# Kernel optimization log

Hardware: AMD Instinct MI355X
Metric: run time of the kernel (lower is better)

Reference implementation:

```python
import jax, jax.numpy as jnp
import numpy as np

DIM = 512
N_DAYS = 24

def setup_inputs() -> dict:
    key = jax.random.key(0)
    k1, k2, k3, k4 = jax.random.split(key, 4)
    x = jax.random.normal(k1, (64, 1024, DIM), dtype=jnp.float32)
    day_ids = jax.random.randint(k2, (64,), 0, N_DAYS, dtype=jnp.int64)
    W = jax.random.normal(k3, (N_DAYS, DIM, DIM), dtype=jnp.float32) * 0.02 + jnp.eye(DIM, dtype=jnp.float32)
    b = jax.random.normal(k4, (N_DAYS, DIM), dtype=jnp.float32) * 0.02
    return {"x": x, "day_ids": day_ids, "W": W, "b": b}

def reference(x, day_ids, W, b):
    # Gather per-sample day weights/biases, batched matmul + bias, softsign.
    # (Dropout is identity in eval mode.)
    Wd = W[day_ids]            # [B, dim, dim]
    bd = b[day_ids][:, None, :]  # [B, 1, dim]
    y = jnp.einsum('btd,bde->bte', x, Wd) + bd
    return y / (1.0 + jnp.abs(y))  # Softsign
```

## Files before the change

kernel.cpp:

```cpp
#include <hip/hip_runtime.h>


#define DIM 512
#define SEQ 1024
#define NB 64
#define NDAYS 24
#define BM 64
#define BN 128
#define BK 64
#define LDA (BK + 8)

typedef __bf16 bf16x8 __attribute__((ext_vector_type(8)));
typedef __bf16 bf16x4 __attribute__((ext_vector_type(4)));
typedef float  f32x4  __attribute__((ext_vector_type(4)));

__device__ __forceinline__ void gll16(const void* g, void* l) {
    __builtin_amdgcn_global_load_lds(
        (const __attribute__((address_space(1))) unsigned int*)g,
        (__attribute__((address_space(3))) unsigned int*)l,
        16, 0, 0);
}

__global__ __launch_bounds__(256)
void transpose_w_kernel(const float* __restrict__ W, __bf16* __restrict__ Wt) {
    __shared__ __bf16 T[32][33];
    const int d  = blockIdx.z;
    const int k0 = blockIdx.x * 32;
    const int n0 = blockIdx.y * 32;
    const int tx = threadIdx.x & 31;
    const int ty = threadIdx.x >> 5;
    const float* Wd = W + (size_t)d * DIM * DIM;
    #pragma unroll
    for (int i = 0; i < 4; ++i) {
        const int k = ty + i * 8;
        T[tx][k] = (__bf16)Wd[(size_t)(k0 + k) * DIM + n0 + tx];
    }
    __syncthreads();
    __bf16* Wtd = Wt + (size_t)d * DIM * DIM;
    #pragma unroll
    for (int i = 0; i < 4; ++i) {
        const int n = ty + i * 8;
        Wtd[(size_t)(n0 + n) * DIM + k0 + tx] = T[n][tx];
    }
}

__global__ __launch_bounds__(256, 5)
void day_adapter_kernel(const float* __restrict__ x,
                        const int*   __restrict__ day_ids,
                        const __bf16* __restrict__ Wt,
                        const float* __restrict__ bias,
                        float*       __restrict__ out)
{
    __shared__ __align__(16) __bf16 As[BM][LDA];
    __shared__ __align__(16) __bf16 Bs[BN * BK];

    const int L  = blockIdx.x;
    const int g  = (L >> 3) & 3;
    const int mb = (L & 7) | ((L >> 5) << 3);
    const int m  = mb & 15;
    const int bb = mb >> 4;

    const int n0  = g * BN;
    const int m0  = m * BM;
    const int tid = threadIdx.x;
    const int day = day_ids[bb];

    const float*  xb  = x   + (size_t)bb  * SEQ * DIM + (size_t)m0 * DIM;
    const __bf16* Wtb = Wt  + (size_t)day * DIM * DIM + (size_t)n0 * DIM;
    float*        ob  = out + (size_t)bb  * SEQ * DIM + (size_t)m0 * DIM + n0;

    const int wave = tid >> 6;
    const int lane = tid & 63;
    const int wm   = (wave >> 1) * 32;
    const int wn   = (wave & 1) * 64;
    const int l15  = lane & 15;
    const int quad = lane >> 4;
    const int kq   = quad * 8;

    const int a_row = tid >> 2;
    const int a_col = (tid & 3) * 4;

    char* BsB = (char*)Bs;

    f32x4 acc[2][4];
    const f32x4 zero = {0.f, 0.f, 0.f, 0.f};
    #pragma unroll
    for (int i = 0; i < 2; ++i)
        #pragma unroll
        for (int j = 0; j < 4; ++j) acc[i][j] = zero;

    for (int kk = 0; kk < DIM; kk += BK) {
        #pragma unroll
        for (int p = 0; p < 4; ++p) {
            const int s  = p * 256 + tid;
            const int n  = s >> 3;
            const int cp = s & 7;
            const int c  = cp ^ (n & 7);
            gll16(Wtb + (size_t)n * DIM + kk + c * 8,
                  BsB + (size_t)(p * 256 + (tid & ~63)) * 16);
        }
        #pragma unroll
        for (int i = 0; i < 4; ++i) {
            const int col = a_col + i * 16;
            const float4 f = *(const float4*)(xb + (size_t)a_row * DIM + kk + col);
            bf16x4 v;
            v[0] = (__bf16)f.x; v[1] = (__bf16)f.y;
            v[2] = (__bf16)f.z; v[3] = (__bf16)f.w;
            *(bf16x4*)&As[a_row][col] = v;
        }
        __syncthreads();

        #pragma unroll
        for (int ks = 0; ks < 2; ++ks) {
            bf16x8 af[2], bfr[4];
            #pragma unroll
            for (int i = 0; i < 2; ++i)
                af[i] = *(const bf16x8*)&As[wm + i * 16 + l15][ks * 32 + kq];
            #pragma unroll
            for (int j = 0; j < 4; ++j) {
                const int n  = wn + j * 16 + l15;
                const int c  = ks * 4 + quad;
                const int cp = c ^ (n & 7);
                bfr[j] = *(const bf16x8*)&Bs[n * BK + cp * 8];
            }
            #pragma unroll
            for (int i = 0; i < 2; ++i)
                #pragma unroll
                for (int j = 0; j < 4; ++j)
                    acc[i][j] = __builtin_amdgcn_mfma_f32_16x16x32_bf16(
                        af[i], bfr[j], acc[i][j], 0, 0, 0);
        }
        __syncthreads();
    }

    float bv[4];
    #pragma unroll
    for (int j = 0; j < 4; ++j)
        bv[j] = bias[(size_t)day * DIM + n0 + wn + j * 16 + l15];

    #pragma unroll
    for (int i = 0; i < 2; ++i) {
        const int rbase = wm + i * 16 + quad * 4;
        #pragma unroll
        for (int j = 0; j < 4; ++j) {
            const int col = wn + j * 16 + l15;
            #pragma unroll
            for (int r = 0; r < 4; ++r) {
                const float y = acc[i][j][r] + bv[j];
                ob[(size_t)(rbase + r) * DIM + col] = y / (1.0f + fabsf(y));
            }
        }
    }
}

extern "C" void kernel_launch(void* const* d_in, const int* in_sizes, int n_in,
                              void* d_out, int out_size, void* d_ws, size_t ws_size,
                              hipStream_t stream) {
    const float* x       = (const float*)d_in[0];
    const int*   day_ids = (const int*)  d_in[1];
    const float* W       = (const float*)d_in[2];
    const float* bias    = (const float*)d_in[3];
    float*       out     = (float*)d_out;
    __bf16*      Wt      = (__bf16*)d_ws;

    dim3 tgrid(DIM / 32, DIM / 32, NDAYS);
    transpose_w_kernel<<<tgrid, 256, 0, stream>>>(W, Wt);

    day_adapter_kernel<<<dim3(4096), 256, 0, stream>>>(x, day_ids, Wt, bias, out);
}
```

Baseline: 310.6 us.

## Keep full weight slice resident in LDS and stream x directly into registers

The GEMM kernel is restructured so each 1024-thread block loads the whole 128x512 bf16 slice of the day's weight into LDS once, using a padded rotated layout, and then covers all 1024 rows of one batch. The x tile is no longer staged through LDS. Each wave loads fp32 x rows straight from global memory, converts them to bf16 fragments, and runs MFMAs with no per-k-step barriers. This removes repeated weight reloads and the per-tile syncthreads. In exchange the grid shrinks to 256 large blocks, and x loads are uncoalesced row fragments whose latency is not hidden by double buffering.

```diff
diff --git a/kernel.cpp b/kernel.cpp
--- a/kernel.cpp
+++ b/kernel.cpp
@@ -3,15 +3,11 @@
 
 #define DIM 512
 #define SEQ 1024
-#define NB 64
 #define NDAYS 24
-#define BM 64
 #define BN 128
-#define BK 64
-#define LDA (BK + 8)
+#define GRAN16 65
 
 typedef __bf16 bf16x8 __attribute__((ext_vector_type(8)));
-typedef __bf16 bf16x4 __attribute__((ext_vector_type(4)));
 typedef float  f32x4  __attribute__((ext_vector_type(4)));
 
 __device__ __forceinline__ void gll16(const void* g, void* l) {
@@ -44,110 +40,90 @@
     }
 }
 
-__global__ __launch_bounds__(256, 5)
+__global__ __launch_bounds__(1024, 4)
 void day_adapter_kernel(const float* __restrict__ x,
                         const int*   __restrict__ day_ids,
                         const __bf16* __restrict__ Wt,
                         const float* __restrict__ bias,
                         float*       __restrict__ out)
 {
-    __shared__ __align__(16) __bf16 As[BM][LDA];
-    __shared__ __align__(16) __bf16 Bs[BN * BK];
+    __shared__ __align__(16) char Bs[BN * GRAN16 * 16];
 
-    const int L  = blockIdx.x;
-    const int g  = (L >> 3) & 3;
-    const int mb = (L & 7) | ((L >> 5) << 3);
-    const int m  = mb & 15;
-    const int bb = mb >> 4;
+    const int L   = blockIdx.x;
+    const int h   = L >> 3;
+    const int g   = h & 3;
+    const int bb  = (L & 7) + 8 * (h >> 2);
 
-    const int n0  = g * BN;
-    const int m0  = m * BM;
-    const int tid = threadIdx.x;
-    const int day = day_ids[bb];
-
-    const float*  xb  = x   + (size_t)bb  * SEQ * DIM + (size_t)m0 * DIM;
-    const __bf16* Wtb = Wt  + (size_t)day * DIM * DIM + (size_t)n0 * DIM;
-    float*        ob  = out + (size_t)bb  * SEQ * DIM + (size_t)m0 * DIM + n0;
-
+    const int tid  = threadIdx.x;
     const int wave = tid >> 6;
     const int lane = tid & 63;
-    const int wm   = (wave >> 1) * 32;
-    const int wn   = (wave & 1) * 64;
     const int l15  = lane & 15;
     const int quad = lane >> 4;
-    const int kq   = quad * 8;
 
-    const int a_row = tid >> 2;
-    const int a_col = (tid & 3) * 4;
+    const int day = day_ids[bb];
+    const __bf16* Wtb = Wt  + (size_t)day * DIM * DIM + (size_t)(g * BN) * DIM;
+    const float*  xb  = x   + (size_t)bb  * SEQ * DIM;
+    float*        ob  = out + (size_t)bb  * SEQ * DIM + g * BN;
+    const float*  bd  = bias + (size_t)day * DIM + g * BN;
 
-    char* BsB = (char*)Bs;
+    #pragma unroll
+    for (int it = 0; it < 8; ++it) {
+        const int n = it * 16 + wave;
+        const int t = (lane - 4 * n) & 63;
+        const int c = ((t & 15) << 2) | (t >> 4);
+        gll16(Wtb + (size_t)n * DIM + c * 8,
+              Bs + n * (GRAN16 * 16));
+    }
+    __syncthreads();
 
-    f32x4 acc[2][4];
-    const f32x4 zero = {0.f, 0.f, 0.f, 0.f};
     #pragma unroll
-    for (int i = 0; i < 2; ++i)
+    for (int ch = 0; ch < 2; ++ch) {
+        const int r0 = wave * 64 + ch * 32;
+
+        f32x4 acc[2][8];
+        const f32x4 zero = {0.f, 0.f, 0.f, 0.f};
         #pragma unroll
-        for (int j = 0; j < 4; ++j) acc[i][j] = zero;
-
-    for (int kk = 0; kk < DIM; kk += BK) {
-        #pragma unroll
-        for (int p = 0; p < 4; ++p) {
-            const int s  = p * 256 + tid;
-            const int n  = s >> 3;
-            const int cp = s & 7;
-            const int c  = cp ^ (n & 7);
-            gll16(Wtb + (size_t)n * DIM + kk + c * 8,
-                  BsB + (size_t)(p * 256 + (tid & ~63)) * 16);
-        }
-        #pragma unroll
-        for (int i = 0; i < 4; ++i) {
-            const int col = a_col + i * 16;
-            const float4 f = *(const float4*)(xb + (size_t)a_row * DIM + kk + col);
-            bf16x4 v;
-            v[0] = (__bf16)f.x; v[1] = (__bf16)f.y;
-            v[2] = (__bf16)f.z; v[3] = (__bf16)f.w;
-            *(bf16x4*)&As[a_row][col] = v;
-        }
-        __syncthreads();
+        for (int i = 0; i < 2; ++i)
+            #pragma unroll
+            for (int j = 0; j < 8; ++j) acc[i][j] = zero;
 
         #pragma unroll
-        for (int ks = 0; ks < 2; ++ks) {
-            bf16x8 af[2], bfr[4];
+        for (int kc = 0; kc < 16; ++kc) {
+            bf16x8 af[2];
             #pragma unroll
-            for (int i = 0; i < 2; ++i)
-                af[i] = *(const bf16x8*)&As[wm + i * 16 + l15][ks * 32 + kq];
-            #pragma unroll
-            for (int j = 0; j < 4; ++j) {
-                const int n  = wn + j * 16 + l15;
-                const int c  = ks * 4 + quad;
-                const int cp = c ^ (n & 7);
-                bfr[j] = *(const bf16x8*)&Bs[n * BK + cp * 8];
+            for (int i = 0; i < 2; ++i) {
+                const float* p = xb + (size_t)(r0 + i * 16 + l15) * DIM
+                                    + kc * 32 + quad * 8;
+                const float4 f0 = *(const float4*)p;
+                const float4 f1 = *(const float4*)(p + 4);
+                bf16x8 v;
+                v[0] = (__bf16)f0.x; v[1] = (__bf16)f0.y;
+                v[2] = (__bf16)f0.z; v[3] = (__bf16)f0.w;
+                v[4] = (__bf16)f1.x; v[5] = (__bf16)f1.y;
+                v[6] = (__bf16)f1.z; v[7] = (__bf16)f1.w;
+                af[i] = v;
             }
             #pragma unroll
-            for (int i = 0; i < 2; ++i)
+            for (int j = 0; j < 8; ++j) {
+                const int n  = j * 16 + l15;
+                const int cp = (quad * 16 + kc + 4 * n) & 63;
+                const bf16x8 bv = *(const bf16x8*)(Bs + n * (GRAN16 * 16) + cp * 16);
+                acc[0][j] = __builtin_amdgcn_mfma_f32_16x16x32_bf16(af[0], bv, acc[0][j], 0, 0, 0);
+                acc[1][j] = __builtin_amdgcn_mfma_f32_16x16x32_bf16(af[1], bv, acc[1][j], 0, 0, 0);
+            }
+        }
+
+        #pragma unroll
+        for (int j = 0; j < 8; ++j) {
+            const float bvj = bd[j * 16 + l15];
+            #pragma unroll
+            for (int i = 0; i < 2; ++i) {
+                const int rbase = r0 + i * 16 + quad * 4;
                 #pragma unroll
-                for (int j = 0; j < 4; ++j)
-                    acc[i][j] = __builtin_amdgcn_mfma_f32_16x16x32_bf16(
-                        af[i], bfr[j], acc[i][j], 0, 0, 0);
-        }
-        __syncthreads();
-    }
-
-    float bv[4];
-    #pragma unroll
-    for (int j = 0; j < 4; ++j)
-        bv[j] = bias[(size_t)day * DIM + n0 + wn + j * 16 + l15];
-
-    #pragma unroll
-    for (int i = 0; i < 2; ++i) {
-        const int rbase = wm + i * 16 + quad * 4;
-        #pragma unroll
-        for (int j = 0; j < 4; ++j) {
-            const int col = wn + j * 16 + l15;
-            #pragma unroll
-            for (int r = 0; r < 4; ++r) {
-                const float y = acc[i][j][r] + bv[j];
-                ob[(size_t)(rbase + r) * DIM + col] = y / (1.0f + fabsf(y));
+                for (int r = 0; r < 4; ++r) {
+                    const float y = acc[i][j][r] + bvj;
+                    ob[(size_t)(rbase + r) * DIM + j * 16 + l15] = y / (1.0f + fabsf(y));
+                }
             }
         }
     }
@@ -166,5 +142,5 @@
     dim3 tgrid(DIM / 32, DIM / 32, NDAYS);
     transpose_w_kernel<<<tgrid, 256, 0, stream>>>(W, Wt);
 
-    day_adapter_kernel<<<dim3(4096), 256, 0, stream>>>(x, day_ids, Wt, bias, out);
+    day_adapter_kernel<<<dim3(256), 1024, 0, stream>>>(x, day_ids, Wt, bias, out);
 }
```

New measurement: 403.0 us. 29.7% more time.
